# Kernel tuning notes

Hardware: AMD Instinct MI355X
Metric: run time of the kernel (lower is better)

The kernel has to match this reference:

```python
import jax, jax.numpy as jnp
import numpy as np

H = 64          # hiddens_dims
K = 3           # Chebyshev order
B = 16          # graphs in batch
NPG = 16384     # nodes per graph
N = B * NPG     # total nodes
E = 2_097_152   # total edges
R = 2191        # num_residues (hard-coded in source)
E_REF = R * 16
HALF = N // 2   # backbone count == sidechain count (mask is balanced per graph)


def _lin(k, fan_in, shape):
    return jax.random.uniform(k, shape, jnp.float32, -1.0, 1.0) / np.sqrt(fan_in)


def setup_inputs() -> dict:
    key = jax.random.key(0)
    ks = jax.random.split(key, 40)
    inp = {}
    inp["x"] = jax.random.normal(ks[0], (N, 3), jnp.float32)
    inp["edge_index"] = jax.random.randint(ks[1], (2, E), 0, N)
    inp["batch"] = jnp.repeat(jnp.arange(B, dtype=jnp.int32), NPG)
    blk = jnp.concatenate([jnp.ones((NPG // 2,), bool), jnp.zeros((NPG // 2,), bool)])
    inp["mask"] = jnp.tile(blk, B)  # backbone=True first half of each graph block
    inp["x_ref"] = jax.random.normal(ks[2], (R, 3), jnp.float32)
    inp["edgeref"] = jax.random.randint(ks[3], (2, E_REF), 0, R)
    i = 4
    for name, cin in [("cw0", 3), ("cw1", H), ("cw2", H), ("rw0", 3), ("rw1", H), ("rw2", H)]:
        inp[name] = _lin(ks[i], cin, (K, cin, H)); i += 1
        inp[name.replace("w", "b")] = jnp.zeros((H,), jnp.float32)  # ChebConv bias init = zeros
    for name, cin, cout in [("mlp_w", 2 * H, H), ("mlpP2_w", 2 * H, H),
                            ("rep0_w", H, H), ("rep1_w", H, H), ("rep2_w", H, 3)]:
        inp[name] = _lin(ks[i], cin, (cin, cout)); i += 1
        inp[name.replace("_w", "_b")] = _lin(ks[i], cin, (cout,)); i += 1
    return inp


def cheb_conv(x, edge_index, W, b, n):
    # PyG ChebConv with sym normalization, lambda_max=2: L_hat = -D^-1/2 A D^-1/2 (diag = 0)
    row, col = edge_index[0], edge_index[1]
    deg = jax.ops.segment_sum(jnp.ones_like(x[:, 0])[row] * 0 + 1.0, row, num_segments=n)
    dinv = jnp.where(deg > 0, jax.lax.rsqrt(jnp.maximum(deg, 1e-12)), 0.0)
    w = -(dinv[row] * dinv[col])  # [E]

    def prop(h):  # L_hat @ h via gather + segment_sum
        return jax.ops.segment_sum(w[:, None] * h[col], row, num_segments=n)

    Tx0 = x
    out = Tx0 @ W[0]
    Tx1 = prop(x)
    out = out + Tx1 @ W[1]
    for k in range(2, K):
        Tx2 = 2.0 * prop(Tx1) - Tx0
        out = out + Tx2 @ W[k]
        Tx0, Tx1 = Tx1, Tx2
    return out + b


def _forward(x, edge_index, mask, x_ref, edgeref,
             cw0, cb0, cw1, cb1, cw2, cb2, rw0, rb0, rw1, rb1, rw2, rb2,
             mlp_w, mlp_b, mlpP2_w, mlpP2_b,
             rep0_w, rep0_b, rep1_w, rep1_b, rep2_w, rep2_b):
    # main GNN stack (tanh after all but last; dropout is identity in eval)
    h = jnp.tanh(cheb_conv(x, edge_index, cw0, cb0, N))
    h = jnp.tanh(cheb_conv(h, edge_index, cw1, cb1, N))
    h = cheb_conv(h, edge_index, cw2, cb2, N)

    bb_idx = jnp.nonzero(mask, size=HALF)[0]
    sc_idx = jnp.nonzero(~mask, size=HALF)[0]
    x_bb = h[bb_idx].reshape(B, -1, H).mean(axis=1)[:, None, :]  # [B,1,H]
    x_sc = h[sc_idx].reshape(B, -1, H).mean(axis=1)[:, None, :]  # [B,1,H]

    # reference-graph stack: source bug makes `conv2 != self.convs[-1]` always True,
    # so tanh follows every convRef layer
    r = jnp.tanh(cheb_conv(x_ref, edgeref, rw0, rb0, R))
    r = jnp.tanh(cheb_conv(r, edgeref, rw1, rb1, R))
    r = jnp.tanh(cheb_conv(r, edgeref, rw2, rb2, R))
    r = jnp.broadcast_to(r[None], (B, R, H))

    bb_rep = jnp.broadcast_to(x_bb, (B, R, H))
    phase1 = jnp.concatenate([r, bb_rep], axis=-1) @ mlp_w + mlp_b        # [B,R,H]
    sc_rep = jnp.broadcast_to(x_sc, (B, R, H))
    phase2 = jnp.concatenate([phase1, sc_rep], axis=-1) @ mlpP2_w + mlpP2_b  # [B,R,H]

    res = phase2.reshape(-1, H)
    res = jax.nn.relu(res @ rep0_w + rep0_b)
    res = jax.nn.relu(res @ rep1_w + rep1_b)
    res = jax.nn.relu(res @ rep2_w + rep2_b)  # [B*R, 3]
    return res.reshape(-1, 3), x_bb, x_sc


def reference(x, edge_index, batch, mask, x_ref, edgeref,
              cw0, cb0, cw1, cb1, cw2, cb2, rw0, rb0, rw1, rb1, rw2, rb2,
              mlp_w, mlp_b, mlpP2_w, mlpP2_b,
              rep0_w, rep0_b, rep1_w, rep1_b, rep2_w, rep2_b):
    del batch  # only used for len(batch.unique()) == B, a static constant here
    return _forward(x, edge_index, mask, x_ref, edgeref,
                    cw0, cb0, cw1, cb1, cw2, cb2, rw0, rb0, rw1, rb1, rw2, rb2,
                    mlp_w, mlp_b, mlpP2_w, mlpP2_b,
                    rep0_w, rep0_b, rep1_w, rep1_b, rep2_w, rep2_b)
```

## Files before the change

kernel.cpp:

```cpp
#include <hip/hip_runtime.h>
#include <hip/hip_fp16.h>
#include <math.h>

#define NN 262144
#define NE 2097152
#define RR 2191
#define ER (RR*16)
#define NB 16
#define BRR (NB*RR)
#define OUT_RES (BRR*3)

typedef __attribute__((ext_vector_type(8))) _Float16 half8;
typedef __attribute__((ext_vector_type(4))) float f32x4;

__global__ void k_hist(const int* __restrict__ row, int* __restrict__ deg, int nE){
  int i = blockIdx.x*blockDim.x + threadIdx.x;
  int st = gridDim.x*blockDim.x;
  for (; i < nE; i += st) atomicAdd(&deg[row[i]], 1);
}

__global__ void k_dinv(const int* __restrict__ deg, float* __restrict__ dinv, int n){
  int i = blockIdx.x*blockDim.x + threadIdx.x;
  if (i < n){ int d = deg[i]; dinv[i] = d > 0 ? 1.0f/sqrtf((float)d) : 0.0f; }
}

__global__ void k_scan1(const int* __restrict__ deg, int* __restrict__ rowptr, int* __restrict__ partials){
  __shared__ int s[256];
  int t = threadIdx.x; int i = blockIdx.x*256 + t;
  int v = deg[i]; s[t] = v; __syncthreads();
  for (int off = 1; off < 256; off <<= 1){
    int x = (t >= off) ? s[t-off] : 0; __syncthreads();
    s[t] += x; __syncthreads();
  }
  rowptr[i] = s[t] - v;
  if (t == 255) partials[blockIdx.x] = s[255];
}

__global__ void k_scan2(int* __restrict__ partials){
  __shared__ int s[1024];
  int t = threadIdx.x; int v = partials[t]; s[t] = v; __syncthreads();
  for (int off = 1; off < 1024; off <<= 1){
    int x = (t >= off) ? s[t-off] : 0; __syncthreads();
    s[t] += x; __syncthreads();
  }
  partials[t] = s[t] - v;
}

__global__ void k_scan3(int* __restrict__ rowptr, const int* __restrict__ partials){
  int t = threadIdx.x; int i = blockIdx.x*256 + t;
  rowptr[i] += partials[blockIdx.x];
  if (i == 0) rowptr[NN] = NE;
}

__global__ void k_scan_small(const int* __restrict__ deg, int* __restrict__ rowptr, int n){
  __shared__ int s[256];
  int t = threadIdx.x;
  int carry = 0;
  for (int base = 0; base < n; base += 256){
    int idx = base + t;
    int v = (idx < n) ? deg[idx] : 0;
    s[t] = v; __syncthreads();
    for (int off = 1; off < 256; off <<= 1){
      int x = (t >= off) ? s[t-off] : 0; __syncthreads();
      s[t] += x; __syncthreads();
    }
    if (idx < n) rowptr[idx] = carry + s[t] - v;
    carry += s[255];
    __syncthreads();
  }
  if (t == 0) rowptr[n] = carry;
}

__global__ void k_scatter(const int* __restrict__ row, const int* __restrict__ col,
                          const float* __restrict__ dinv, const int* __restrict__ rowptr,
                          int* __restrict__ cursor, int2* __restrict__ pair, int nE){
  int i = blockIdx.x*blockDim.x + threadIdx.x;
  int st = gridDim.x*blockDim.x;
  for (; i < nE; i += st){
    int r = row[i], c = col[i];
    int pos = rowptr[r] + atomicAdd(&cursor[r], 1);
    pair[pos] = make_int2(c, __float_as_int(-dinv[r]*dinv[c]));
  }
}

__global__ void k_prop3(const float* __restrict__ h, float* __restrict__ y,
                        const int* __restrict__ rowptr, const int2* __restrict__ pair, int n){
  int i = blockIdx.x*blockDim.x + threadIdx.x;
  if (i >= n) return;
  float a0 = 0.f, a1 = 0.f, a2 = 0.f;
  int s = rowptr[i], e = rowptr[i+1];
  int p = s;
  for (; p + 4 <= e; p += 4){
    int2 q0 = pair[p], q1 = pair[p+1], q2 = pair[p+2], q3 = pair[p+3];
    float w0 = __int_as_float(q0.y), w1 = __int_as_float(q1.y);
    float w2 = __int_as_float(q2.y), w3 = __int_as_float(q3.y);
    float x00=h[q0.x*3+0], x01=h[q0.x*3+1], x02=h[q0.x*3+2];
    float x10=h[q1.x*3+0], x11=h[q1.x*3+1], x12=h[q1.x*3+2];
    float x20=h[q2.x*3+0], x21=h[q2.x*3+1], x22=h[q2.x*3+2];
    float x30=h[q3.x*3+0], x31=h[q3.x*3+1], x32=h[q3.x*3+2];
    a0 = fmaf(w0,x00, fmaf(w1,x10, fmaf(w2,x20, fmaf(w3,x30, a0))));
    a1 = fmaf(w0,x01, fmaf(w1,x11, fmaf(w2,x21, fmaf(w3,x31, a1))));
    a2 = fmaf(w0,x02, fmaf(w1,x12, fmaf(w2,x22, fmaf(w3,x32, a2))));
  }
  for (; p < e; p++){
    int2 q = pair[p]; float wv = __int_as_float(q.y);
    a0 = fmaf(wv, h[q.x*3+0], a0); a1 = fmaf(wv, h[q.x*3+1], a1); a2 = fmaf(wv, h[q.x*3+2], a2);
  }
  y[i*3+0] = a0; y[i*3+1] = a1; y[i*3+2] = a2;
}

__global__ void k_prop64(const float* __restrict__ h, float* __restrict__ y,
                         const int* __restrict__ rowptr, const int2* __restrict__ pair, int n){
  int t = threadIdx.x, lane = t & 63;
  int i = blockIdx.x*4 + (t >> 6);
  if (i >= n) return;
  float acc = 0.f;
  int s = rowptr[i], e = rowptr[i+1];
  int p = s;
  for (; p + 4 <= e; p += 4){
    int2 q0 = pair[p], q1 = pair[p+1], q2 = pair[p+2], q3 = pair[p+3];
    float v0 = h[(size_t)q0.x*64 + lane], v1 = h[(size_t)q1.x*64 + lane];
    float v2 = h[(size_t)q2.x*64 + lane], v3 = h[(size_t)q3.x*64 + lane];
    acc = fmaf(__int_as_float(q0.y),v0, fmaf(__int_as_float(q1.y),v1,
          fmaf(__int_as_float(q2.y),v2, fmaf(__int_as_float(q3.y),v3, acc))));
  }
  for (; p < e; p++){
    int2 q = pair[p];
    acc = fmaf(__int_as_float(q.y), h[(size_t)q.x*64 + lane], acc);
  }
  y[(size_t)i*64 + lane] = acc;
}

__global__ void __launch_bounds__(256) k_prop64h(
    const uint2* __restrict__ h2, uint2* __restrict__ y2,
    const int* __restrict__ rowptr, const int2* __restrict__ pair, int n){
  int t = threadIdx.x;
  int sub = t & 15;
  int row = blockIdx.x*16 + (t >> 4);
  if (row >= n) return;
  int s = rowptr[row], e = rowptr[row+1];
  float a0=0.f, a1=0.f, a2=0.f, a3=0.f;
  int p = s;
  for (; p + 4 <= e; p += 4){
    int2 q0 = pair[p], q1 = pair[p+1], q2 = pair[p+2], q3 = pair[p+3];
    uint2 v0 = h2[(size_t)q0.x*16 + sub];
    uint2 v1 = h2[(size_t)q1.x*16 + sub];
    uint2 v2 = h2[(size_t)q2.x*16 + sub];
    uint2 v3 = h2[(size_t)q3.x*16 + sub];
    float w0 = __int_as_float(q0.y), w1 = __int_as_float(q1.y);
    float w2 = __int_as_float(q2.y), w3 = __int_as_float(q3.y);
    float2 f0a = __half22float2(*(__half2*)&v0.x), f0b = __half22float2(*(__half2*)&v0.y);
    float2 f1a = __half22float2(*(__half2*)&v1.x), f1b = __half22float2(*(__half2*)&v1.y);
    float2 f2a = __half22float2(*(__half2*)&v2.x), f2b = __half22float2(*(__half2*)&v2.y);
    float2 f3a = __half22float2(*(__half2*)&v3.x), f3b = __half22float2(*(__half2*)&v3.y);
    a0 = fmaf(w0,f0a.x, fmaf(w1,f1a.x, fmaf(w2,f2a.x, fmaf(w3,f3a.x, a0))));
    a1 = fmaf(w0,f0a.y, fmaf(w1,f1a.y, fmaf(w2,f2a.y, fmaf(w3,f3a.y, a1))));
    a2 = fmaf(w0,f0b.x, fmaf(w1,f1b.x, fmaf(w2,f2b.x, fmaf(w3,f3b.x, a2))));
    a3 = fmaf(w0,f0b.y, fmaf(w1,f1b.y, fmaf(w2,f2b.y, fmaf(w3,f3b.y, a3))));
  }
  for (; p < e; p++){
    int2 q = pair[p];
    float wv = __int_as_float(q.y);
    uint2 v = h2[(size_t)q.x*16 + sub];
    float2 fa = __half22float2(*(__half2*)&v.x), fb = __half22float2(*(__half2*)&v.y);
    a0 = fmaf(wv, fa.x, a0); a1 = fmaf(wv, fa.y, a1);
    a2 = fmaf(wv, fb.x, a2); a3 = fmaf(wv, fb.y, a3);
  }
  __half2 lo = __floats2half2_rn(a0, a1), hi = __floats2half2_rn(a2, a3);
  uint2 r; r.x = *(unsigned*)&lo; r.y = *(unsigned*)&hi;
  y2[(size_t)row*16 + sub] = r;
}

__global__ void k_combine3f(const float* __restrict__ x, const float* __restrict__ t1,
                            const float* __restrict__ t2, const float* __restrict__ W,
                            const float* __restrict__ bias, float* __restrict__ out, int n){
  int t = threadIdx.x, lane = t & 63;
  int i = blockIdx.x*4 + (t >> 6);
  if (i >= n) return;
  float acc = bias[lane];
  #pragma unroll
  for (int j = 0; j < 3; j++){
    float x0 = x[i*3+j], x1 = t1[i*3+j];
    float x2 = 2.0f*t2[i*3+j] - x0;
    acc += x0*W[      j*64 + lane]
         + x1*W[192 + j*64 + lane]
         + x2*W[384 + j*64 + lane];
  }
  out[(size_t)i*64 + lane] = tanhf(acc);
}

__global__ void k_combine3h(const float* __restrict__ x, const float* __restrict__ t1,
                            const float* __restrict__ t2, const float* __restrict__ W,
                            const float* __restrict__ bias, __half* __restrict__ out, int n){
  int t = threadIdx.x, lane = t & 63;
  int i = blockIdx.x*4 + (t >> 6);
  if (i >= n) return;
  float acc = bias[lane];
  #pragma unroll
  for (int j = 0; j < 3; j++){
    float x0 = x[i*3+j], x1 = t1[i*3+j];
    float x2 = 2.0f*t2[i*3+j] - x0;
    acc += x0*W[      j*64 + lane]
         + x1*W[192 + j*64 + lane]
         + x2*W[384 + j*64 + lane];
  }
  out[(size_t)i*64 + lane] = __float2half_rn(tanhf(acc));
}

__global__ void k_weff(const float* __restrict__ W, float* __restrict__ D){
  int i = blockIdx.x*blockDim.x + threadIdx.x;
  D[i]        = W[i] - W[8192 + i];
  D[4096 + i] = W[4096 + i];
  D[8192 + i] = 2.0f * W[8192 + i];
}

__global__ void k_wpack(const float* __restrict__ W, _Float16* __restrict__ D){
  int t = blockIdx.x*blockDim.x + threadIdx.x;
  int reg = t & 7, lane = (t >> 3) & 63, nt = (t >> 9) & 3, kc = t >> 11;
  int m = kc >> 1;
  int kin = (kc & 1)*32 + ((lane >> 4) & 3)*8 + reg;
  int n = nt*16 + (lane & 15);
  float eff;
  if      (m == 0) eff = W[kin*64 + n] - W[8192 + kin*64 + n];
  else if (m == 1) eff = W[4096 + kin*64 + n];
  else             eff = 2.0f * W[8192 + kin*64 + n];
  D[t] = (_Float16)eff;
}

__global__ void __launch_bounds__(256) k_combine64m(
    const __half* A, const __half* B, const __half* C,
    const _Float16* __restrict__ wfrag, const float* __restrict__ bias,
    __half* out, int ntiles, int wavestride){
  int t = threadIdx.x;
  int lane = t & 63;
  int wv = blockIdx.x*4 + (t >> 6);
  half8 bf[24];
  #pragma unroll
  for (int i = 0; i < 24; i++)
    bf[i] = *(const half8*)(wfrag + ((size_t)(i*64 + lane))*8);
  int col = lane & 15, grp = (lane >> 4) & 3;
  float b0 = bias[col], b1 = bias[16+col], b2 = bias[32+col], b3 = bias[48+col];
  for (int tile = wv; tile < ntiles; tile += wavestride){
    size_t rb = (size_t)tile*16;
    f32x4 acc0 = {b0,b0,b0,b0}, acc1 = {b1,b1,b1,b1};
    f32x4 acc2 = {b2,b2,b2,b2}, acc3 = {b3,b3,b3,b3};
    #pragma unroll
    for (int kc = 0; kc < 6; kc++){
      const __half* s = (kc < 2) ? A : (kc < 4) ? B : C;
      half8 a = *(const half8*)(s + (rb + col)*64 + (kc & 1)*32 + grp*8);
      acc0 = __builtin_amdgcn_mfma_f32_16x16x32_f16(a, bf[kc*4+0], acc0, 0,0,0);
      acc1 = __builtin_amdgcn_mfma_f32_16x16x32_f16(a, bf[kc*4+1], acc1, 0,0,0);
      acc2 = __builtin_amdgcn_mfma_f32_16x16x32_f16(a, bf[kc*4+2], acc2, 0,0,0);
      acc3 = __builtin_amdgcn_mfma_f32_16x16x32_f16(a, bf[kc*4+3], acc3, 0,0,0);
    }
    __half* o = out + (rb + grp*4)*64;
    #pragma unroll
    for (int r = 0; r < 4; r++){
      o[(size_t)r*64 +      col] = __float2half_rn(tanhf(acc0[r]));
      o[(size_t)r*64 + 16 + col] = __float2half_rn(tanhf(acc1[r]));
      o[(size_t)r*64 + 32 + col] = __float2half_rn(tanhf(acc2[r]));
      o[(size_t)r*64 + 48 + col] = __float2half_rn(tanhf(acc3[r]));
    }
  }
}

__global__ void k_pool3(const __half2* __restrict__ hA, const __half2* __restrict__ hB,
                        const __half2* __restrict__ hC, float* __restrict__ pA,
                        float* __restrict__ pB, float* __restrict__ pC){
  const __half2* src = (blockIdx.y == 0) ? hA : (blockIdx.y == 1) ? hB : hC;
  float* dst         = (blockIdx.y == 0) ? pA : (blockIdx.y == 1) ? pB : pC;
  int blk = blockIdx.x;
  int chunk = blk & 15, seg = blk >> 4;
  int t = threadIdx.x, ch2 = t & 31, rsub = t >> 5;
  int base = seg*8192 + chunk*512;
  float ax = 0.f, ay = 0.f;
  for (int j = 0; j < 64; j++){
    int row = base + rsub + j*8;
    float2 v = __half22float2(src[(size_t)row*32 + ch2]);
    ax += v.x; ay += v.y;
  }
  __shared__ float sx[256], sy[256];
  sx[t] = ax; sy[t] = ay; __syncthreads();
  if (t < 32){
    float tx = 0.f, ty = 0.f;
    #pragma unroll
    for (int j = 0; j < 8; j++){ tx += sx[ch2 + j*32]; ty += sy[ch2 + j*32]; }
    int b = seg >> 1, half_ = seg & 1;
    atomicAdd(&dst[half_*1024 + b*64 + ch2*2],     tx);
    atomicAdd(&dst[half_*1024 + b*64 + ch2*2 + 1], ty);
  }
}

__global__ void k_combine_pooled(const float* __restrict__ pA, const float* __restrict__ pB,
                                 const float* __restrict__ pC, const float* __restrict__ weff,
                                 const float* __restrict__ bias, float* __restrict__ xbbsc,
                                 float* __restrict__ dout){
  int i = blockIdx.x*blockDim.x + threadIdx.x;
  int pr = i >> 6, c = i & 63;
  const float* a = pA + pr*64;
  const float* b = pB + pr*64;
  const float* cc = pC + pr*64;
  float v = 0.f;
  for (int k = 0; k < 64; k++){
    v = fmaf(a[k],  weff[        k*64 + c], v);
    v = fmaf(b[k],  weff[4096 +  k*64 + c], v);
    v = fmaf(cc[k], weff[8192 +  k*64 + c], v);
  }
  v = v*(1.0f/8192.0f) + bias[c];
  xbbsc[i] = v;
  dout[OUT_RES + i] = v;
}

__global__ void __launch_bounds__(256) k_combine64f(
    const float* __restrict__ A, const float* __restrict__ Bm, const float* __restrict__ C,
    const float* __restrict__ Weff, const float* __restrict__ bias,
    float* __restrict__ out, int n){
  int t = threadIdx.x;
  int lane = t & 63;
  int wid  = __builtin_amdgcn_readfirstlane(t >> 6);
  int half_ = wid & 1;
  int row  = blockIdx.x*128 + (wid >> 1)*64 + lane;
  bool active = (row < n);
  float acc[32];
  #pragma unroll
  for (int c = 0; c < 32; c++) acc[c] = bias[half_*32 + c];
  if (active){
    #pragma unroll 1
    for (int m = 0; m < 3; m++){
      const float* src = (m == 0 ? A : (m == 1 ? Bm : C)) + (size_t)row*64;
      const float* Wm  = Weff + m*4096 + half_*32;
      #pragma unroll 1
      for (int k4 = 0; k4 < 16; k4++){
        float4 a4 = *(const float4*)(src + k4*4);
        const float* wk = Wm + k4*256;
        #pragma unroll
        for (int kk = 0; kk < 4; kk++){
          float a = (kk == 0) ? a4.x : (kk == 1) ? a4.y : (kk == 2) ? a4.z : a4.w;
          #pragma unroll
          for (int c = 0; c < 32; c++)
            acc[c] = fmaf(a, wk[kk*64 + c], acc[c]);
        }
      }
    }
  }
  __syncthreads();
  if (active){
    float* o = out + (size_t)row*64 + half_*32;
    #pragma unroll
    for (int c = 0; c < 32; c++) o[c] = tanhf(acc[c]);
  }
}

__global__ void k_matrows(const float* __restrict__ in, const float* __restrict__ W,
                          const float* __restrict__ bias, float* __restrict__ out,
                          int n, int accum){
  int t = threadIdx.x, lane = t & 63;
  int i = blockIdx.x*4 + (t >> 6);
  if (i >= n) return;
  float v = in[i*64 + lane];
  float acc = bias ? bias[lane] : 0.0f;
  #pragma unroll
  for (int k = 0; k < 64; k++) acc += __shfl(v, k, 64) * W[k*64 + lane];
  if (accum) acc += out[i*64 + lane];
  out[i*64 + lane] = acc;
}

__global__ void k_final(const float* __restrict__ rt3, const float* __restrict__ bt3,
                        const float* __restrict__ W1, const float* __restrict__ b1,
                        const float* __restrict__ W2, const float* __restrict__ b2,
                        float* __restrict__ dout){
  int t = threadIdx.x, lane = t & 63;
  int g = blockIdx.x*4 + (t >> 6);
  if (g >= BRR) return;
  int b = g / RR, r = g - b*RR;
  float m = rt3[r*64 + lane] + bt3[b*64 + lane];
  m = fmaxf(m, 0.0f);
  float acc = b1[lane];
  #pragma unroll
  for (int k = 0; k < 64; k++) acc += __shfl(m, k, 64) * W1[k*64 + lane];
  float u = fmaxf(acc, 0.0f);
  float p0 = u*W2[lane*3+0], p1 = u*W2[lane*3+1], p2 = u*W2[lane*3+2];
  #pragma unroll
  for (int off = 32; off > 0; off >>= 1){
    p0 += __shfl_xor(p0, off, 64);
    p1 += __shfl_xor(p1, off, 64);
    p2 += __shfl_xor(p2, off, 64);
  }
  if (lane == 0){
    dout[g*3+0] = fmaxf(p0 + b2[0], 0.0f);
    dout[g*3+1] = fmaxf(p1 + b2[1], 0.0f);
    dout[g*3+2] = fmaxf(p2 + b2[2], 0.0f);
  }
}

extern "C" void kernel_launch(void* const* d_in, const int* in_sizes, int n_in,
                              void* d_out, int out_size, void* d_ws, size_t ws_size,
                              hipStream_t stream){
  const float* x     = (const float*)d_in[0];
  const int*   eidx  = (const int*)d_in[1];
  const float* x_ref = (const float*)d_in[4];
  const int*   eref  = (const int*)d_in[5];
  const float* cw0 = (const float*)d_in[6],  *cb0 = (const float*)d_in[7];
  const float* cw1 = (const float*)d_in[8],  *cb1 = (const float*)d_in[9];
  const float* cw2 = (const float*)d_in[10], *cb2 = (const float*)d_in[11];
  const float* rw0 = (const float*)d_in[12], *rb0 = (const float*)d_in[13];
  const float* rw1 = (const float*)d_in[14], *rb1 = (const float*)d_in[15];
  const float* rw2 = (const float*)d_in[16], *rb2 = (const float*)d_in[17];
  const float* mlp_w  = (const float*)d_in[18], *mlp_b  = (const float*)d_in[19];
  const float* mlp2_w = (const float*)d_in[20], *mlp2_b = (const float*)d_in[21];
  const float* rep0_w = (const float*)d_in[22], *rep0_b = (const float*)d_in[23];
  const float* rep1_w = (const float*)d_in[24], *rep1_b = (const float*)d_in[25];
  const float* rep2_w = (const float*)d_in[26], *rep2_b = (const float*)d_in[27];
  float* out = (float*)d_out;

  char* w = (char*)d_ws;
  size_t off = 0;
  auto alloc = [&](size_t bytes)->void*{
    void* p = w + off;
    off = (off + bytes + 255) & ~(size_t)255;
    return p;
  };
  int*   deg     = (int*)  alloc(NN*4);
  int*   cursor  = (int*)  alloc(NN*4);
  int*   degR    = (int*)  alloc(RR*4);
  int*   cursorR = (int*)  alloc(RR*4);
  float* poolA   = (float*)alloc(2048*4);
  float* poolB   = (float*)alloc(2048*4);
  float* poolC   = (float*)alloc(2048*4);
  size_t zero_bytes = off;

  int*   rowptr   = (int*)  alloc((NN+1)*4);
  int*   partials = (int*)  alloc(1024*4);
  int*   rowptrR  = (int*)  alloc((RR+1)*4);
  float* dinv     = (float*)alloc(NN*4);
  float* dinvR    = (float*)alloc(RR*4);
  int2*  cpair    = (int2*) alloc((size_t)NE*8);
  int2*  cpairR   = (int2*) alloc((size_t)ER*8);
  float* t1_3     = (float*)alloc((size_t)NN*3*4);
  float* t2_3     = (float*)alloc((size_t)NN*3*4);
  float* rt1_3    = (float*)alloc(RR*3*4);
  float* rt2_3    = (float*)alloc(RR*3*4);
  __half* hA      = (__half*)alloc((size_t)NN*64*2);
  __half* hB      = (__half*)alloc((size_t)NN*64*2);
  __half* hC      = (__half*)alloc((size_t)NN*64*2);
  float* refA     = (float*)alloc(RR*64*4);
  float* refB     = (float*)alloc(RR*64*4);
  float* refC     = (float*)alloc(RR*64*4);
  float* xbbsc    = (float*)alloc(2048*4);
  float* rterm    = (float*)alloc(RR*64*4);
  float* bbterm   = (float*)alloc(NB*64*4);
  float* rt2a     = (float*)alloc(RR*64*4);
  float* bt2a     = (float*)alloc(NB*64*4);
  float* rt3a     = (float*)alloc(RR*64*4);
  float* bt3a     = (float*)alloc(NB*64*4);
  float* weffC2   = (float*)alloc(12288*4);
  float* weffR1   = (float*)alloc(12288*4);
  float* weffR2   = (float*)alloc(12288*4);
  _Float16* wfragC1 = (_Float16*)alloc(12288*2);
  (void)ws_size; (void)in_sizes; (void)n_in; (void)out_size;

  hipMemsetAsync(d_ws, 0, zero_bytes, stream);

  k_weff<<<16, 256, 0, stream>>>(cw2, weffC2);
  k_weff<<<16, 256, 0, stream>>>(rw1, weffR1);
  k_weff<<<16, 256, 0, stream>>>(rw2, weffR2);
  k_wpack<<<48, 256, 0, stream>>>(cw1, wfragC1);

  k_hist<<<2048, 256, 0, stream>>>(eidx, deg, NE);
  k_hist<<<64,   256, 0, stream>>>(eref, degR, ER);
  k_dinv<<<1024, 256, 0, stream>>>(deg, dinv, NN);
  k_dinv<<<9,    256, 0, stream>>>(degR, dinvR, RR);
  k_scan1<<<1024, 256, 0, stream>>>(deg, rowptr, partials);
  k_scan2<<<1, 1024, 0, stream>>>(partials);
  k_scan3<<<1024, 256, 0, stream>>>(rowptr, partials);
  k_scan_small<<<1, 256, 0, stream>>>(degR, rowptrR, RR);
  k_scatter<<<2048, 256, 0, stream>>>(eidx, eidx+NE, dinv, rowptr, cursor, cpair, NE);
  k_scatter<<<64,   256, 0, stream>>>(eref, eref+ER, dinvR, rowptrR, cursorR, cpairR, ER);

  k_prop3<<<1024, 256, 0, stream>>>(x, t1_3, rowptr, cpair, NN);
  k_prop3<<<1024, 256, 0, stream>>>(t1_3, t2_3, rowptr, cpair, NN);
  k_combine3h<<<NN/4, 256, 0, stream>>>(x, t1_3, t2_3, cw0, cb0, hA, NN);
  k_prop64h<<<NN/16, 256, 0, stream>>>((const uint2*)hA, (uint2*)hB, rowptr, cpair, NN);
  k_prop64h<<<NN/16, 256, 0, stream>>>((const uint2*)hB, (uint2*)hC, rowptr, cpair, NN);
  k_combine64m<<<1024, 256, 0, stream>>>(hA, hB, hC, wfragC1, cb1, hA, NN/16, 4096);
  k_prop64h<<<NN/16, 256, 0, stream>>>((const uint2*)hA, (uint2*)hB, rowptr, cpair, NN);
  k_prop64h<<<NN/16, 256, 0, stream>>>((const uint2*)hB, (uint2*)hC, rowptr, cpair, NN);
  k_pool3<<<dim3(512,3), 256, 0, stream>>>((const __half2*)hA, (const __half2*)hB,
                                           (const __half2*)hC, poolA, poolB, poolC);
  k_combine_pooled<<<8, 256, 0, stream>>>(poolA, poolB, poolC, weffC2, cb2, xbbsc, out);

  k_prop3<<<9, 256, 0, stream>>>(x_ref, rt1_3, rowptrR, cpairR, RR);
  k_prop3<<<9, 256, 0, stream>>>(rt1_3, rt2_3, rowptrR, cpairR, RR);
  k_combine3f<<<548, 256, 0, stream>>>(x_ref, rt1_3, rt2_3, rw0, rb0, refA, RR);
  k_prop64<<<548, 256, 0, stream>>>(refA, refB, rowptrR, cpairR, RR);
  k_prop64<<<548, 256, 0, stream>>>(refB, refC, rowptrR, cpairR, RR);
  k_combine64f<<<(RR+127)/128, 256, 0, stream>>>(refA, refB, refC, weffR1, rb1, refA, RR);
  k_prop64<<<548, 256, 0, stream>>>(refA, refB, rowptrR, cpairR, RR);
  k_prop64<<<548, 256, 0, stream>>>(refB, refC, rowptrR, cpairR, RR);
  k_combine64f<<<(RR+127)/128, 256, 0, stream>>>(refA, refB, refC, weffR2, rb2, refA, RR);

  k_matrows<<<548, 256, 0, stream>>>(refA,   mlp_w,        nullptr, rterm,  RR, 0);
  k_matrows<<<4,   256, 0, stream>>>(xbbsc,  mlp_w+4096,   mlp_b,   bbterm, NB, 0);
  k_matrows<<<548, 256, 0, stream>>>(rterm,  mlp2_w,       nullptr, rt2a,   RR, 0);
  k_matrows<<<4,   256, 0, stream>>>(bbterm, mlp2_w,       nullptr, bt2a,   NB, 0);
  k_matrows<<<4,   256, 0, stream>>>(xbbsc+1024, mlp2_w+4096, mlp2_b, bt2a, NB, 1);
  k_matrows<<<548, 256, 0, stream>>>(rt2a,   rep0_w,       nullptr, rt3a,   RR, 0);
  k_matrows<<<4,   256, 0, stream>>>(bt2a,   rep0_w,       rep0_b,  bt3a,   NB, 0);

  k_final<<<(BRR+3)/4, 256, 0, stream>>>(rt3a, bt3a, rep1_w, rep1_b, rep2_w, rep2_b, out);
}
```

Baseline: 760.1 us.

## Store column-only CSR, apply degree normalization on the fly, fuse MLP chains

Edge weights are no longer stored per edge. The CSR holds only column indices, and each propagation looks up dinv[col] and scales the sum by -dinv[row] at the end. This halves edge-array traffic in the scatter and prop kernels at the cost of an extra gather of dinv. The dinv computation is folded into the scan kernels, the 64-wide prop loop is unrolled to 8, and seven small matrow launches are fused into two chain kernels.

```diff
diff --git a/kernel.cpp b/kernel.cpp
--- a/kernel.cpp
+++ b/kernel.cpp
@@ -19,15 +19,12 @@
   for (; i < nE; i += st) atomicAdd(&deg[row[i]], 1);
 }
 
-__global__ void k_dinv(const int* __restrict__ deg, float* __restrict__ dinv, int n){
-  int i = blockIdx.x*blockDim.x + threadIdx.x;
-  if (i < n){ int d = deg[i]; dinv[i] = d > 0 ? 1.0f/sqrtf((float)d) : 0.0f; }
-}
-
-__global__ void k_scan1(const int* __restrict__ deg, int* __restrict__ rowptr, int* __restrict__ partials){
+__global__ void k_scan1(const int* __restrict__ deg, int* __restrict__ rowptr,
+                        int* __restrict__ partials, float* __restrict__ dinv){
   __shared__ int s[256];
   int t = threadIdx.x; int i = blockIdx.x*256 + t;
   int v = deg[i]; s[t] = v; __syncthreads();
+  dinv[i] = v > 0 ? 1.0f/sqrtf((float)v) : 0.0f;
   for (int off = 1; off < 256; off <<= 1){
     int x = (t >= off) ? s[t-off] : 0; __syncthreads();
     s[t] += x; __syncthreads();
@@ -52,13 +49,15 @@
   if (i == 0) rowptr[NN] = NE;
 }
 
-__global__ void k_scan_small(const int* __restrict__ deg, int* __restrict__ rowptr, int n){
+__global__ void k_scan_small(const int* __restrict__ deg, int* __restrict__ rowptr,
+                             float* __restrict__ dinv, int n){
   __shared__ int s[256];
   int t = threadIdx.x;
   int carry = 0;
   for (int base = 0; base < n; base += 256){
     int idx = base + t;
     int v = (idx < n) ? deg[idx] : 0;
+    if (idx < n) dinv[idx] = v > 0 ? 1.0f/sqrtf((float)v) : 0.0f;
     s[t] = v; __syncthreads();
     for (int off = 1; off < 256; off <<= 1){
       int x = (t >= off) ? s[t-off] : 0; __syncthreads();
@@ -72,101 +71,117 @@
 }
 
 __global__ void k_scatter(const int* __restrict__ row, const int* __restrict__ col,
-                          const float* __restrict__ dinv, const int* __restrict__ rowptr,
-                          int* __restrict__ cursor, int2* __restrict__ pair, int nE){
+                          const int* __restrict__ rowptr, int* __restrict__ cursor,
+                          int* __restrict__ csr_col, int nE){
   int i = blockIdx.x*blockDim.x + threadIdx.x;
   int st = gridDim.x*blockDim.x;
   for (; i < nE; i += st){
-    int r = row[i], c = col[i];
+    int r = row[i];
     int pos = rowptr[r] + atomicAdd(&cursor[r], 1);
-    pair[pos] = make_int2(c, __float_as_int(-dinv[r]*dinv[c]));
+    csr_col[pos] = col[i];
   }
 }
 
 __global__ void k_prop3(const float* __restrict__ h, float* __restrict__ y,
-                        const int* __restrict__ rowptr, const int2* __restrict__ pair, int n){
+                        const int* __restrict__ rowptr, const int* __restrict__ cols,
+                        const float* __restrict__ dinv, int n){
   int i = blockIdx.x*blockDim.x + threadIdx.x;
   if (i >= n) return;
+  float di = dinv[i];
   float a0 = 0.f, a1 = 0.f, a2 = 0.f;
   int s = rowptr[i], e = rowptr[i+1];
   int p = s;
   for (; p + 4 <= e; p += 4){
-    int2 q0 = pair[p], q1 = pair[p+1], q2 = pair[p+2], q3 = pair[p+3];
-    float w0 = __int_as_float(q0.y), w1 = __int_as_float(q1.y);
-    float w2 = __int_as_float(q2.y), w3 = __int_as_float(q3.y);
-    float x00=h[q0.x*3+0], x01=h[q0.x*3+1], x02=h[q0.x*3+2];
-    float x10=h[q1.x*3+0], x11=h[q1.x*3+1], x12=h[q1.x*3+2];
-    float x20=h[q2.x*3+0], x21=h[q2.x*3+1], x22=h[q2.x*3+2];
-    float x30=h[q3.x*3+0], x31=h[q3.x*3+1], x32=h[q3.x*3+2];
+    int c0 = cols[p], c1 = cols[p+1], c2 = cols[p+2], c3 = cols[p+3];
+    float w0 = dinv[c0], w1 = dinv[c1], w2 = dinv[c2], w3 = dinv[c3];
+    float x00=h[c0*3+0], x01=h[c0*3+1], x02=h[c0*3+2];
+    float x10=h[c1*3+0], x11=h[c1*3+1], x12=h[c1*3+2];
+    float x20=h[c2*3+0], x21=h[c2*3+1], x22=h[c2*3+2];
+    float x30=h[c3*3+0], x31=h[c3*3+1], x32=h[c3*3+2];
     a0 = fmaf(w0,x00, fmaf(w1,x10, fmaf(w2,x20, fmaf(w3,x30, a0))));
     a1 = fmaf(w0,x01, fmaf(w1,x11, fmaf(w2,x21, fmaf(w3,x31, a1))));
     a2 = fmaf(w0,x02, fmaf(w1,x12, fmaf(w2,x22, fmaf(w3,x32, a2))));
   }
   for (; p < e; p++){
-    int2 q = pair[p]; float wv = __int_as_float(q.y);
-    a0 = fmaf(wv, h[q.x*3+0], a0); a1 = fmaf(wv, h[q.x*3+1], a1); a2 = fmaf(wv, h[q.x*3+2], a2);
-  }
-  y[i*3+0] = a0; y[i*3+1] = a1; y[i*3+2] = a2;
+    int c = cols[p]; float wv = dinv[c];
+    a0 = fmaf(wv, h[c*3+0], a0); a1 = fmaf(wv, h[c*3+1], a1); a2 = fmaf(wv, h[c*3+2], a2);
+  }
+  y[i*3+0] = -di*a0; y[i*3+1] = -di*a1; y[i*3+2] = -di*a2;
 }
 
 __global__ void k_prop64(const float* __restrict__ h, float* __restrict__ y,
-                         const int* __restrict__ rowptr, const int2* __restrict__ pair, int n){
+                         const int* __restrict__ rowptr, const int* __restrict__ cols,
+                         const float* __restrict__ dinv, int n){
   int t = threadIdx.x, lane = t & 63;
   int i = blockIdx.x*4 + (t >> 6);
   if (i >= n) return;
+  float di = dinv[i];
   float acc = 0.f;
   int s = rowptr[i], e = rowptr[i+1];
   int p = s;
   for (; p + 4 <= e; p += 4){
-    int2 q0 = pair[p], q1 = pair[p+1], q2 = pair[p+2], q3 = pair[p+3];
-    float v0 = h[(size_t)q0.x*64 + lane], v1 = h[(size_t)q1.x*64 + lane];
-    float v2 = h[(size_t)q2.x*64 + lane], v3 = h[(size_t)q3.x*64 + lane];
-    acc = fmaf(__int_as_float(q0.y),v0, fmaf(__int_as_float(q1.y),v1,
-          fmaf(__int_as_float(q2.y),v2, fmaf(__int_as_float(q3.y),v3, acc))));
-  }
-  for (; p < e; p++){
-    int2 q = pair[p];
-    acc = fmaf(__int_as_float(q.y), h[(size_t)q.x*64 + lane], acc);
-  }
-  y[(size_t)i*64 + lane] = acc;
+    int c0 = cols[p], c1 = cols[p+1], c2 = cols[p+2], c3 = cols[p+3];
+    float v0 = h[(size_t)c0*64 + lane], v1 = h[(size_t)c1*64 + lane];
+    float v2 = h[(size_t)c2*64 + lane], v3 = h[(size_t)c3*64 + lane];
+    acc = fmaf(dinv[c0],v0, fmaf(dinv[c1],v1, fmaf(dinv[c2],v2, fmaf(dinv[c3],v3, acc))));
+  }
+  for (; p < e; p++) acc = fmaf(dinv[cols[p]], h[(size_t)cols[p]*64 + lane], acc);
+  y[(size_t)i*64 + lane] = -di*acc;
 }
 
 __global__ void __launch_bounds__(256) k_prop64h(
     const uint2* __restrict__ h2, uint2* __restrict__ y2,
-    const int* __restrict__ rowptr, const int2* __restrict__ pair, int n){
+    const int* __restrict__ rowptr, const int* __restrict__ cols,
+    const float* __restrict__ dinv, int n){
   int t = threadIdx.x;
   int sub = t & 15;
   int row = blockIdx.x*16 + (t >> 4);
   if (row >= n) return;
   int s = rowptr[row], e = rowptr[row+1];
+  float di = dinv[row];
   float a0=0.f, a1=0.f, a2=0.f, a3=0.f;
   int p = s;
+  for (; p + 8 <= e; p += 8){
+    int c[8]; uint2 v[8]; float wv[8];
+    #pragma unroll
+    for (int j = 0; j < 8; j++) c[j] = cols[p+j];
+    #pragma unroll
+    for (int j = 0; j < 8; j++) v[j] = h2[(size_t)c[j]*16 + sub];
+    #pragma unroll
+    for (int j = 0; j < 8; j++) wv[j] = dinv[c[j]];
+    #pragma unroll
+    for (int j = 0; j < 8; j++){
+      float2 fa = __half22float2(*(__half2*)&v[j].x);
+      float2 fb = __half22float2(*(__half2*)&v[j].y);
+      a0 = fmaf(wv[j], fa.x, a0); a1 = fmaf(wv[j], fa.y, a1);
+      a2 = fmaf(wv[j], fb.x, a2); a3 = fmaf(wv[j], fb.y, a3);
+    }
+  }
   for (; p + 4 <= e; p += 4){
-    int2 q0 = pair[p], q1 = pair[p+1], q2 = pair[p+2], q3 = pair[p+3];
-    uint2 v0 = h2[(size_t)q0.x*16 + sub];
-    uint2 v1 = h2[(size_t)q1.x*16 + sub];
-    uint2 v2 = h2[(size_t)q2.x*16 + sub];
-    uint2 v3 = h2[(size_t)q3.x*16 + sub];
-    float w0 = __int_as_float(q0.y), w1 = __int_as_float(q1.y);
-    float w2 = __int_as_float(q2.y), w3 = __int_as_float(q3.y);
-    float2 f0a = __half22float2(*(__half2*)&v0.x), f0b = __half22float2(*(__half2*)&v0.y);
-    float2 f1a = __half22float2(*(__half2*)&v1.x), f1b = __half22float2(*(__half2*)&v1.y);
-    float2 f2a = __half22float2(*(__half2*)&v2.x), f2b = __half22float2(*(__half2*)&v2.y);
-    float2 f3a = __half22float2(*(__half2*)&v3.x), f3b = __half22float2(*(__half2*)&v3.y);
-    a0 = fmaf(w0,f0a.x, fmaf(w1,f1a.x, fmaf(w2,f2a.x, fmaf(w3,f3a.x, a0))));
-    a1 = fmaf(w0,f0a.y, fmaf(w1,f1a.y, fmaf(w2,f2a.y, fmaf(w3,f3a.y, a1))));
-    a2 = fmaf(w0,f0b.x, fmaf(w1,f1b.x, fmaf(w2,f2b.x, fmaf(w3,f3b.x, a2))));
-    a3 = fmaf(w0,f0b.y, fmaf(w1,f1b.y, fmaf(w2,f2b.y, fmaf(w3,f3b.y, a3))));
+    int c[4]; uint2 v[4]; float wv[4];
+    #pragma unroll
+    for (int j = 0; j < 4; j++) c[j] = cols[p+j];
+    #pragma unroll
+    for (int j = 0; j < 4; j++) v[j] = h2[(size_t)c[j]*16 + sub];
+    #pragma unroll
+    for (int j = 0; j < 4; j++) wv[j] = dinv[c[j]];
+    #pragma unroll
+    for (int j = 0; j < 4; j++){
+      float2 fa = __half22float2(*(__half2*)&v[j].x);
+      float2 fb = __half22float2(*(__half2*)&v[j].y);
+      a0 = fmaf(wv[j], fa.x, a0); a1 = fmaf(wv[j], fa.y, a1);
+      a2 = fmaf(wv[j], fb.x, a2); a3 = fmaf(wv[j], fb.y, a3);
+    }
   }
   for (; p < e; p++){
-    int2 q = pair[p];
-    float wv = __int_as_float(q.y);
-    uint2 v = h2[(size_t)q.x*16 + sub];
+    int c = cols[p];
+    float wv = dinv[c];
+    uint2 v = h2[(size_t)c*16 + sub];
     float2 fa = __half22float2(*(__half2*)&v.x), fb = __half22float2(*(__half2*)&v.y);
     a0 = fmaf(wv, fa.x, a0); a1 = fmaf(wv, fa.y, a1);
     a2 = fmaf(wv, fb.x, a2); a3 = fmaf(wv, fb.y, a3);
   }
-  __half2 lo = __floats2half2_rn(a0, a1), hi = __floats2half2_rn(a2, a3);
+  __half2 lo = __floats2half2_rn(-di*a0, -di*a1), hi = __floats2half2_rn(-di*a2, -di*a3);
   uint2 r; r.x = *(unsigned*)&lo; r.y = *(unsigned*)&hi;
   y2[(size_t)row*16 + sub] = r;
 }
@@ -351,18 +366,47 @@
   }
 }
 
-__global__ void k_matrows(const float* __restrict__ in, const float* __restrict__ W,
-                          const float* __restrict__ bias, float* __restrict__ out,
-                          int n, int accum){
+__global__ void k_refchain(const float* __restrict__ refA, const float* __restrict__ mlp_w,
+                           const float* __restrict__ mlp2_w, const float* __restrict__ rep0_w,
+                           float* __restrict__ rt3a, int n){
   int t = threadIdx.x, lane = t & 63;
   int i = blockIdx.x*4 + (t >> 6);
   if (i >= n) return;
-  float v = in[i*64 + lane];
-  float acc = bias ? bias[lane] : 0.0f;
-  #pragma unroll
-  for (int k = 0; k < 64; k++) acc += __shfl(v, k, 64) * W[k*64 + lane];
-  if (accum) acc += out[i*64 + lane];
-  out[i*64 + lane] = acc;
+  float v = refA[i*64 + lane];
+  float a = 0.f;
+  #pragma unroll
+  for (int k = 0; k < 64; k++) a += __shfl(v, k, 64) * mlp_w[k*64 + lane];
+  float b = 0.f;
+  #pragma unroll
+  for (int k = 0; k < 64; k++) b += __shfl(a, k, 64) * mlp2_w[k*64 + lane];
+  float c = 0.f;
+  #pragma unroll
+  for (int k = 0; k < 64; k++) c += __shfl(b, k, 64) * rep0_w[k*64 + lane];
+  rt3a[i*64 + lane] = c;
+}
+
+__global__ void k_bbchain(const float* __restrict__ xbbsc,
+                          const float* __restrict__ mlp_w,  const float* __restrict__ mlp_b,
+                          const float* __restrict__ mlp2_w, const float* __restrict__ mlp2_b,
+                          const float* __restrict__ rep0_w, const float* __restrict__ rep0_b,
+                          float* __restrict__ bt3a){
+  int t = threadIdx.x, lane = t & 63;
+  int i = blockIdx.x*4 + (t >> 6);
+  if (i >= NB) return;
+  float vbb = xbbsc[i*64 + lane];
+  float vsc = xbbsc[1024 + i*64 + lane];
+  float a = mlp_b[lane];
+  #pragma unroll
+  for (int k = 0; k < 64; k++) a += __shfl(vbb, k, 64) * mlp_w[4096 + k*64 + lane];
+  float b = mlp2_b[lane];
+  #pragma unroll
+  for (int k = 0; k < 64; k++) b += __shfl(a, k, 64) * mlp2_w[k*64 + lane];
+  #pragma unroll
+  for (int k = 0; k < 64; k++) b += __shfl(vsc, k, 64) * mlp2_w[4096 + k*64 + lane];
+  float c = rep0_b[lane];
+  #pragma unroll
+  for (int k = 0; k < 64; k++) c += __shfl(b, k, 64) * rep0_w[k*64 + lane];
+  bt3a[i*64 + lane] = c;
 }
 
 __global__ void k_final(const float* __restrict__ rt3, const float* __restrict__ bt3,
@@ -434,8 +478,8 @@
   int*   rowptrR  = (int*)  alloc((RR+1)*4);
   float* dinv     = (float*)alloc(NN*4);
   float* dinvR    = (float*)alloc(RR*4);
-  int2*  cpair    = (int2*) alloc((size_t)NE*8);
-  int2*  cpairR   = (int2*) alloc((size_t)ER*8);
+  int*   csr_col  = (int*)  alloc((size_t)NE*4);
+  int*   csr_colR = (int*)  alloc((size_t)ER*4);
   float* t1_3     = (float*)alloc((size_t)NN*3*4);
   float* t2_3     = (float*)alloc((size_t)NN*3*4);
   float* rt1_3    = (float*)alloc(RR*3*4);
@@ -447,10 +491,6 @@
   float* refB     = (float*)alloc(RR*64*4);
   float* refC     = (float*)alloc(RR*64*4);
   float* xbbsc    = (float*)alloc(2048*4);
-  float* rterm    = (float*)alloc(RR*64*4);
-  float* bbterm   = (float*)alloc(NB*64*4);
-  float* rt2a     = (float*)alloc(RR*64*4);
-  float* bt2a     = (float*)alloc(NB*64*4);
   float* rt3a     = (float*)alloc(RR*64*4);
   float* bt3a     = (float*)alloc(NB*64*4);
   float* weffC2   = (float*)alloc(12288*4);
@@ -468,44 +508,37 @@
 
   k_hist<<<2048, 256, 0, stream>>>(eidx, deg, NE);
   k_hist<<<64,   256, 0, stream>>>(eref, degR, ER);
-  k_dinv<<<1024, 256, 0, stream>>>(deg, dinv, NN);
-  k_dinv<<<9,    256, 0, stream>>>(degR, dinvR, RR);
-  k_scan1<<<1024, 256, 0, stream>>>(deg, rowptr, partials);
+  k_scan1<<<1024, 256, 0, stream>>>(deg, rowptr, partials, dinv);
   k_scan2<<<1, 1024, 0, stream>>>(partials);
   k_scan3<<<1024, 256, 0, stream>>>(rowptr, partials);
-  k_scan_small<<<1, 256, 0, stream>>>(degR, rowptrR, RR);
-  k_scatter<<<2048, 256, 0, stream>>>(eidx, eidx+NE, dinv, rowptr, cursor, cpair, NE);
-  k_scatter<<<64,   256, 0, stream>>>(eref, eref+ER, dinvR, rowptrR, cursorR, cpairR, ER);
-
-  k_prop3<<<1024, 256, 0, stream>>>(x, t1_3, rowptr, cpair, NN);
-  k_prop3<<<1024, 256, 0, stream>>>(t1_3, t2_3, rowptr, cpair, NN);
+  k_scan_small<<<1, 256, 0, stream>>>(degR, rowptrR, dinvR, RR);
+  k_scatter<<<2048, 256, 0, stream>>>(eidx, eidx+NE, rowptr, cursor, csr_col, NE);
+  k_scatter<<<64,   256, 0, stream>>>(eref, eref+ER, rowptrR, cursorR, csr_colR, ER);
+
+  k_prop3<<<1024, 256, 0, stream>>>(x, t1_3, rowptr, csr_col, dinv, NN);
+  k_prop3<<<1024, 256, 0, stream>>>(t1_3, t2_3, rowptr, csr_col, dinv, NN);
   k_combine3h<<<NN/4, 256, 0, stream>>>(x, t1_3, t2_3, cw0, cb0, hA, NN);
-  k_prop64h<<<NN/16, 256, 0, stream>>>((const uint2*)hA, (uint2*)hB, rowptr, cpair, NN);
-  k_prop64h<<<NN/16, 256, 0, stream>>>((const uint2*)hB, (uint2*)hC, rowptr, cpair, NN);
+  k_prop64h<<<NN/16, 256, 0, stream>>>((const uint2*)hA, (uint2*)hB, rowptr, csr_col, dinv, NN);
+  k_prop64h<<<NN/16, 256, 0, stream>>>((const uint2*)hB, (uint2*)hC, rowptr, csr_col, dinv, NN);
   k_combine64m<<<1024, 256, 0, stream>>>(hA, hB, hC, wfragC1, cb1, hA, NN/16, 4096);
-  k_prop64h<<<NN/16, 256, 0, stream>>>((const uint2*)hA, (uint2*)hB, rowptr, cpair, NN);
-  k_prop64h<<<NN/16, 256, 0, stream>>>((const uint2*)hB, (uint2*)hC, rowptr, cpair, NN);
+  k_prop64h<<<NN/16, 256, 0, stream>>>((const uint2*)hA, (uint2*)hB, rowptr, csr_col, dinv, NN);
+  k_prop64h<<<NN/16, 256, 0, stream>>>((const uint2*)hB, (uint2*)hC, rowptr, csr_col, dinv, NN);
   k_pool3<<<dim3(512,3), 256, 0, stream>>>((const __half2*)hA, (const __half2*)hB,
                                            (const __half2*)hC, poolA, poolB, poolC);
   k_combine_pooled<<<8, 256, 0, stream>>>(poolA, poolB, poolC, weffC2, cb2, xbbsc, out);
 
-  k_prop3<<<9, 256, 0, stream>>>(x_ref, rt1_3, rowptrR, cpairR, RR);
-  k_prop3<<<9, 256, 0, stream>>>(rt1_3, rt2_3, rowptrR, cpairR, RR);
+  k_prop3<<<9, 256, 0, stream>>>(x_ref, rt1_3, rowptrR, csr_colR, dinvR, RR);
+  k_prop3<<<9, 256, 0, stream>>>(rt1_3, rt2_3, rowptrR, csr_colR, dinvR, RR);
   k_combine3f<<<548, 256, 0, stream>>>(x_ref, rt1_3, rt2_3, rw0, rb0, refA, RR);
-  k_prop64<<<548, 256, 0, stream>>>(refA, refB, rowptrR, cpairR, RR);
-  k_prop64<<<548, 256, 0, stream>>>(refB, refC, rowptrR, cpairR, RR);
+  k_prop64<<<548, 256, 0, stream>>>(refA, refB, rowptrR, csr_colR, dinvR, RR);
+  k_prop64<<<548, 256, 0, stream>>>(refB, refC, rowptrR, csr_colR, dinvR, RR);
   k_combine64f<<<(RR+127)/128, 256, 0, stream>>>(refA, refB, refC, weffR1, rb1, refA, RR);
-  k_prop64<<<548, 256, 0, stream>>>(refA, refB, rowptrR, cpairR, RR);
-  k_prop64<<<548, 256, 0, stream>>>(refB, refC, rowptrR, cpairR, RR);
+  k_prop64<<<548, 256, 0, stream>>>(refA, refB, rowptrR, csr_colR, dinvR, RR);
+  k_prop64<<<548, 256, 0, stream>>>(refB, refC, rowptrR, csr_colR, dinvR, RR);
   k_combine64f<<<(RR+127)/128, 256, 0, stream>>>(refA, refB, refC, weffR2, rb2, refA, RR);
 
-  k_matrows<<<548, 256, 0, stream>>>(refA,   mlp_w,        nullptr, rterm,  RR, 0);
-  k_matrows<<<4,   256, 0, stream>>>(xbbsc,  mlp_w+4096,   mlp_b,   bbterm, NB, 0);
-  k_matrows<<<548, 256, 0, stream>>>(rterm,  mlp2_w,       nullptr, rt2a,   RR, 0);
-  k_matrows<<<4,   256, 0, stream>>>(bbterm, mlp2_w,       nullptr, bt2a,   NB, 0);
-  k_matrows<<<4,   256, 0, stream>>>(xbbsc+1024, mlp2_w+4096, mlp2_b, bt2a, NB, 1);
-  k_matrows<<<548, 256, 0, stream>>>(rt2a,   rep0_w,       nullptr, rt3a,   RR, 0);
-  k_matrows<<<4,   256, 0, stream>>>(bt2a,   rep0_w,       rep0_b,  bt3a,   NB, 0);
+  k_refchain<<<548, 256, 0, stream>>>(refA, mlp_w, mlp2_w, rep0_w, rt3a, RR);
+  k_bbchain<<<4, 256, 0, stream>>>(xbbsc, mlp_w, mlp_b, mlp2_w, mlp2_b, rep0_w, rep0_b, bt3a);
 
   k_final<<<(BRR+3)/4, 256, 0, stream>>>(rt3a, bt3a, rep1_w, rep1_b, rep2_w, rep2_b, out);
 }
```

Result: slower. 870.0 us (+14.5%).
